# Optimization experiments

Measured on AMD Instinct MI355X. Metric: run time of the kernel, lower is better.

## Reference

```python
import jax, jax.numpy as jnp
import numpy as np
import math

NUM_HEADS = 16
ATTN_WIDTH = 256


def setup_inputs() -> dict:
    key = jax.random.key(0)
    ks = jax.random.split(key, 5)
    B, S, C, H = 2, 2048, 1024, 1024
    scale = 0.02
    return {
        "x": jax.random.normal(ks[0], (B, S, C), dtype=jnp.float32),
        "Wq": jax.random.normal(ks[1], (C, H), dtype=jnp.float32) * scale,
        "Wk": jax.random.normal(ks[2], (C, H), dtype=jnp.float32) * scale,
        "Wv": jax.random.normal(ks[3], (C, H), dtype=jnp.float32) * scale,
        "Wo": jax.random.normal(ks[4], (H, C), dtype=jnp.float32) * scale,
    }


def reference(x, Wq, Wk, Wv, Wo):
    B, S, C = x.shape
    H = NUM_HEADS
    dh = Wq.shape[1] // H  # head dim; Q.size(-1) in torch code

    def split_heads(t):
        # [B, S, H*dh] -> [B, H, S, dh]
        return t.reshape(B, S, H, dh).transpose(0, 2, 1, 3)

    q = split_heads(x @ Wq)
    k = split_heads(x @ Wk)
    v = split_heads(x @ Wv)

    scores = jnp.einsum("bhqd,bhkd->bhqk", q, k) / math.sqrt(dh)
    # exp-shift (first 'softmax-like' step, unnormalized)
    scores = jnp.exp(scores - jnp.max(scores, axis=-1, keepdims=True))
    # banded mask: tril(attn_width//2 - 1).triu(-(attn_width//2))
    i = jnp.arange(S)[:, None]
    j = jnp.arange(S)[None, :]
    d = j - i
    half = ATTN_WIDTH // 2
    mask = (d <= half - 1) & (d >= -half)
    scores = jnp.where(mask, scores, 0.0)
    # second softmax over the masked exp-scores (zeros contribute exp(0)=1)
    weights = jax.nn.softmax(scores, axis=-1)

    out = jnp.einsum("bhqk,bhkd->bhqd", weights, v)  # [B, H, S, dh]
    out = out.transpose(0, 2, 1, 3).reshape(B, S, H * dh)
    return out @ Wo
```

## Files before the change

### kernel.cpp

```cpp
#include <hip/hip_runtime.h>
#include <math.h>

typedef __bf16 bf16_t;
typedef bf16_t bf16x8 __attribute__((ext_vector_type(8)));
typedef bf16_t bf16x4 __attribute__((ext_vector_type(4)));
typedef float f32x4 __attribute__((ext_vector_type(4)));

constexpr int S_ = 2048;
constexpr float SCALE = 0.125f;

#define MFMA_B16(a, b, c) __builtin_amdgcn_mfma_f32_16x16x32_bf16(a, b, c, 0, 0, 0)

#define WAIT_VM0() __builtin_amdgcn_s_waitcnt(0x0F70)
#define WAIT_VM2() __builtin_amdgcn_s_waitcnt(0x0F72)
#define WAIT_VM4() __builtin_amdgcn_s_waitcnt(0x0F74)
#define BARRIER()  __builtin_amdgcn_s_barrier()

typedef __attribute__((address_space(1))) const void* as1_cvp;
typedef __attribute__((address_space(3))) void* as3_vp;

__device__ __forceinline__ void gl2lds16(const void* g, void* l)
{
    __builtin_amdgcn_global_load_lds((as1_cvp)g, (as3_vp)l, 16, 0, 0);
}

#define SRC_SWZ8(lane) ((((lane) & 3) ^ (((lane) >> 3) & 3)) * 8)
#define RD_SWZ8(quad, l15) ((((quad) ^ (((l15) >> 1) & 3))) * 8)

__global__ __launch_bounds__(256) void prep(const float* __restrict__ x,
                                            const float* __restrict__ Wq,
                                            const float* __restrict__ Wk,
                                            const float* __restrict__ Wv,
                                            const float* __restrict__ Wo,
                                            bf16_t* __restrict__ xb,
                                            bf16_t* __restrict__ Wqt,
                                            bf16_t* __restrict__ Wkt,
                                            bf16_t* __restrict__ Wvt,
                                            bf16_t* __restrict__ Wot,
                                            float* __restrict__ vsp)
{
    __shared__ float T[64][65];
    const int blk = blockIdx.x;
    const int tid = threadIdx.x;
    if (blk < 1024) {
#pragma unroll
        for (int u = 0; u < 4; ++u) {
            const int g = blk * 1024 + u * 256 + tid;
            const float4 v = ((const float4*)x)[g];
            bf16x4 o;
            o[0] = (bf16_t)v.x; o[1] = (bf16_t)v.y;
            o[2] = (bf16_t)v.z; o[3] = (bf16_t)v.w;
            *(bf16x4*)&xb[(size_t)g * 4] = o;
        }
    } else if (blk < 2048) {
        const int rem = blk - 1024;
        const int wsel = rem >> 8, t = rem & 255;
        const float* src = (wsel == 0) ? Wq : (wsel == 1) ? Wk : (wsel == 2) ? Wv : Wo;
        bf16_t* dst = (wsel == 0) ? Wqt : (wsel == 1) ? Wkt : (wsel == 2) ? Wvt : Wot;
        const int k0 = (t >> 4) * 64, n0 = (t & 15) * 64;
        const int rr = tid >> 4, c4 = (tid & 15) * 4;
#pragma unroll
        for (int u = 0; u < 4; ++u) {
            const float4 v = *(const float4*)&src[(size_t)(k0 + u * 16 + rr) * 1024 + n0 + c4];
            T[u * 16 + rr][c4 + 0] = v.x; T[u * 16 + rr][c4 + 1] = v.y;
            T[u * 16 + rr][c4 + 2] = v.z; T[u * 16 + rr][c4 + 3] = v.w;
        }
        __syncthreads();
#pragma unroll
        for (int u = 0; u < 4; ++u) {
            bf16x4 o;
#pragma unroll
            for (int e = 0; e < 4; ++e) o[e] = (bf16_t)T[c4 + e][u * 16 + rr];
            *(bf16x4*)&dst[(size_t)(n0 + u * 16 + rr) * 1024 + k0 + c4] = o;
        }
    } else {
#pragma unroll
        for (int u = 0; u < 8; ++u) vsp[u * 256 + tid] = 0.f;
    }
}

template <int MODE>
__device__ __forceinline__ void mfma_gemm_body(bf16_t* __restrict__ As,
                                               bf16_t* __restrict__ Bs,
                                               const bf16_t* __restrict__ A,
                                               const bf16_t* __restrict__ Bt,
                                               void* __restrict__ dst,
                                               float* __restrict__ vsum_out,
                                               int m0, int n0)
{
    const int tid = threadIdx.x;
    const int lane = tid & 63, wid = tid >> 6;
    const int l15 = lane & 15, quad = lane >> 4;
    const int wm = (wid & 1) * 64, wn = (wid >> 1) * 64;

    const int srow = wid * 32 + (lane >> 2);
    const int scg8 = SRC_SWZ8(lane);
    const bf16_t* Ag0 = A  + (size_t)(m0 + srow) * 1024 + scg8;
    const bf16_t* Ag1 = A  + (size_t)(m0 + srow + 16) * 1024 + scg8;
    const bf16_t* Bg0 = Bt + (size_t)(n0 + srow) * 1024 + scg8;
    const bf16_t* Bg1 = Bt + (size_t)(n0 + srow + 16) * 1024 + scg8;

    const int rs = RD_SWZ8(quad, l15);

    f32x4 acc[4][4];
#pragma unroll
    for (int i = 0; i < 4; ++i)
#pragma unroll
        for (int j = 0; j < 4; ++j) acc[i][j] = (f32x4){0.f, 0.f, 0.f, 0.f};

#pragma unroll
    for (int p = 0; p < 2; ++p) {
        const int k0 = p * 32;
        gl2lds16(Ag0 + k0, As + p * 4096 + (wid * 2 + 0) * 512);
        gl2lds16(Ag1 + k0, As + p * 4096 + (wid * 2 + 1) * 512);
        gl2lds16(Bg0 + k0, Bs + p * 4096 + (wid * 2 + 0) * 512);
        gl2lds16(Bg1 + k0, Bs + p * 4096 + (wid * 2 + 1) * 512);
    }

#pragma unroll
    for (int it = 0; it < 32; ++it) {
        if (it < 30) WAIT_VM4(); else WAIT_VM0();
        BARRIER();
        if (it < 30) {
            const int k0 = (it + 2) * 32;
            const int sb = (it + 2) % 3;
            gl2lds16(Ag0 + k0, As + sb * 4096 + (wid * 2 + 0) * 512);
            gl2lds16(Ag1 + k0, As + sb * 4096 + (wid * 2 + 1) * 512);
            gl2lds16(Bg0 + k0, Bs + sb * 4096 + (wid * 2 + 0) * 512);
            gl2lds16(Bg1 + k0, Bs + sb * 4096 + (wid * 2 + 1) * 512);
        }
        const int cb = it % 3;
        bf16x8 af[4], bfr[4];
#pragma unroll
        for (int mt = 0; mt < 4; ++mt)
            af[mt] = *(const bf16x8*)&As[cb * 4096 + (wm + mt * 16 + l15) * 32 + rs];
#pragma unroll
        for (int nt = 0; nt < 4; ++nt)
            bfr[nt] = *(const bf16x8*)&Bs[cb * 4096 + (wn + nt * 16 + l15) * 32 + rs];
#pragma unroll
        for (int mt = 0; mt < 4; ++mt)
#pragma unroll
            for (int nt = 0; nt < 4; ++nt)
                acc[mt][nt] = MFMA_B16(bfr[nt], af[mt], acc[mt][nt]);
    }

#pragma unroll
    for (int mt = 0; mt < 4; ++mt) {
        const int m = m0 + wm + mt * 16 + l15;
#pragma unroll
        for (int nt = 0; nt < 4; ++nt) {
            const int nb = n0 + wn + nt * 16 + quad * 4;
            if (MODE == 0) {
                *(f32x4*)&((float*)dst)[(size_t)m * 1024 + nb] = acc[mt][nt];
            } else if (MODE == 1) {
                const int bb = m >> 11, s = m & 2047;
                const int hh = nb >> 6, d = nb & 63;
                bf16x4 o;
#pragma unroll
                for (int u = 0; u < 4; ++u) o[u] = (bf16_t)acc[mt][nt][u];
                *(bf16x4*)&((bf16_t*)dst)[((size_t)(bb * 16 + hh) * 2048 + s) * 64 + d] = o;
            } else {
                const int bb = n0 >> 11;
                const int hh = m >> 6, dd = m & 63;
                bf16x4 o;
#pragma unroll
                for (int u = 0; u < 4; ++u) o[u] = (bf16_t)acc[mt][nt][u];
                *(bf16x4*)&((bf16_t*)dst)[((size_t)(bb * 16 + hh) * 64 + dd) * 2048 + (nb & 2047)] = o;
            }
        }
    }

    if (MODE == 2 && vsum_out != nullptr) {
        const int bb = n0 >> 11;
#pragma unroll
        for (int mt = 0; mt < 4; ++mt) {
            float p = 0.f;
#pragma unroll
            for (int nt = 0; nt < 4; ++nt)
                p += acc[mt][nt][0] + acc[mt][nt][1] + acc[mt][nt][2] + acc[mt][nt][3];
            p += __shfl_xor(p, 16);
            p += __shfl_xor(p, 32);
            if (quad == 0) {
                const int m = m0 + wm + mt * 16 + l15;
                atomicAdd(&vsum_out[(bb * 16 + (m >> 6)) * 64 + (m & 63)], p);
            }
        }
    }
}

__device__ __forceinline__ int remap_m(void) { return (blockIdx.x << 2) + (blockIdx.y >> 3); }
__device__ __forceinline__ int remap_n(void) { return blockIdx.y & 7; }

__global__ __launch_bounds__(256) void gemm_qkv_mfma(const bf16_t* __restrict__ xb,
                                                     const bf16_t* __restrict__ Wqt,
                                                     const bf16_t* __restrict__ Wkt,
                                                     const bf16_t* __restrict__ Wvt,
                                                     bf16_t* Qh, bf16_t* Kh, bf16_t* VhT,
                                                     float* vsp)
{
    __shared__ bf16_t As[12288];
    __shared__ bf16_t Bs[12288];
    if (blockIdx.z == 2) {
        mfma_gemm_body<2>(As, Bs, Wvt, xb, VhT, vsp, remap_n() * 128, remap_m() * 128);
    } else {
        const bf16_t* Bt = (blockIdx.z == 0) ? Wqt : Wkt;
        bf16_t* dst = (blockIdx.z == 0) ? Qh : Kh;
        mfma_gemm_body<1>(As, Bs, xb, Bt, dst, nullptr, remap_m() * 128, remap_n() * 128);
    }
}

__global__ __launch_bounds__(256) void gemm_out_mfma(const bf16_t* __restrict__ attn,
                                                     const bf16_t* __restrict__ Wot,
                                                     float* __restrict__ out)
{
    __shared__ bf16_t As[12288];
    __shared__ bf16_t Bs[12288];
    mfma_gemm_body<0>(As, Bs, attn, Wot, out, nullptr, remap_m() * 128, remap_n() * 128);
}

__global__ __launch_bounds__(256) void attn_k(const bf16_t* __restrict__ Qh,
                                              const bf16_t* __restrict__ Kh,
                                              const bf16_t* __restrict__ VhT,
                                              const float* __restrict__ vsp,
                                              bf16_t* __restrict__ attn)
{
    __shared__ bf16_t Qs[8192];
    __shared__ float mr_sh[128];
    __shared__ __align__(16) char uni[35328];

    float*  msh = (float*)uni;
    bf16_t* Ks2 = (bf16_t*)uni;
    bf16_t* VtL = (bf16_t*)(uni + 8192);
    bf16_t* Ws  = (bf16_t*)(uni + 16384);
    float*  zsh = (float*)(uni + 34816);

    const int tid = threadIdx.x;
    const int lane = tid & 63, wid = tid >> 6;
    const int l15 = lane & 15, quad = lane >> 4;

    const int f = blockIdx.x;
    const int seq = f >> 3;
    const int bh = (f & 7) + 8 * (seq >> 4);
    const int i0 = (seq & 15) * 128;
    const int b = bh >> 4, h = bh & 15;
    const bf16_t* Qb  = Qh  + (size_t)bh * 131072;
    const bf16_t* Kb  = Kh  + (size_t)bh * 131072;
    const bf16_t* VbT = VhT + (size_t)bh * 131072;

    const int ssw = SRC_SWZ8(lane);
    const int rs  = RD_SWZ8(quad, l15);

#pragma unroll
    for (int c = 0; c < 4; ++c) {
        const int gg = wid * 4 + c;
        const int half = gg >> 3;
        const int row = (gg & 7) * 16 + (lane >> 2);
        gl2lds16(Qb + (size_t)(i0 + row) * 64 + half * 32 + ssw, Qs + gg * 512);
    }
    __syncthreads();

    bf16x8 af[8][2];
#pragma unroll
    for (int mt = 0; mt < 8; ++mt)
#pragma unroll
        for (int ks = 0; ks < 2; ++ks)
            af[mt][ks] = *(const bf16x8*)&Qs[ks * 4096 + (mt * 16 + l15) * 32 + rs];

    float vm[8];
#pragma unroll
    for (int mt = 0; mt < 8; ++mt) vm[mt] = -3.0e38f;

    const bf16_t* kf0 = Kb + (size_t)(wid * 16 + l15) * 64 + quad * 8;
    bf16x8 k0 = *(const bf16x8*)(kf0);
    bf16x8 k1 = *(const bf16x8*)(kf0 + 32);

    for (int jc = 0; jc < 32; ++jc) {
        const bf16_t* pn = kf0 + (size_t)((jc < 31) ? (jc + 1) : 31) * 4096;
        const bf16x8 n0 = *(const bf16x8*)(pn);
        const bf16x8 n1 = *(const bf16x8*)(pn + 32);
        __builtin_amdgcn_s_setprio(1);
#pragma unroll
        for (int mt = 0; mt < 8; ++mt) {
            f32x4 t = (f32x4){0.f, 0.f, 0.f, 0.f};
            t = MFMA_B16(k0, af[mt][0], t);
            t = MFMA_B16(k1, af[mt][1], t);
            const float u = fmaxf(fmaxf(t[0], t[1]), t[2]);
            vm[mt] = fmaxf(fmaxf(u, t[3]), vm[mt]);
        }
        __builtin_amdgcn_s_setprio(0);
        k0 = n0; k1 = n1;
    }

#pragma unroll
    for (int mt = 0; mt < 8; ++mt) {
        float v = vm[mt];
        v = fmaxf(v, __shfl_xor(v, 16));
        v = fmaxf(v, __shfl_xor(v, 32));
        if (quad == 0) msh[(wid * 8 + mt) * 16 + l15] = v;
    }
    __syncthreads();

    if (tid < 128) {
        const int mt = tid >> 4, il = tid & 15;
        const float v = fmaxf(fmaxf(msh[(0 * 8 + mt) * 16 + il], msh[(1 * 8 + mt) * 16 + il]),
                              fmaxf(msh[(2 * 8 + mt) * 16 + il], msh[(3 * 8 + mt) * 16 + il]));
        mr_sh[tid] = v * SCALE;
    }
    __syncthreads();

    bf16x8 aq[2][2];
#pragma unroll
    for (int t = 0; t < 2; ++t)
#pragma unroll
        for (int ks = 0; ks < 2; ++ks)
            aq[t][ks] = *(const bf16x8*)&Qs[ks * 4096 + ((wid * 2 + t) * 16 + l15) * 32 + rs];

    float mreg[2][4];
#pragma unroll
    for (int t = 0; t < 2; ++t)
#pragma unroll
        for (int r = 0; r < 4; ++r)
            mreg[t][r] = mr_sh[(wid * 2 + t) * 16 + quad * 4 + r];

    f32x4 vsd4[4];
#pragma unroll
    for (int dt = 0; dt < 4; ++dt)
        vsd4[dt] = *(const f32x4*)&vsp[bh * 64 + dt * 16 + quad * 4];

    f32x4 accO[2][4];
#pragma unroll
    for (int t = 0; t < 2; ++t)
#pragma unroll
        for (int dt = 0; dt < 4; ++dt) accO[t][dt] = (f32x4){0.f, 0.f, 0.f, 0.f};
    float zp[2][4] = {{0.f, 0.f, 0.f, 0.f}, {0.f, 0.f, 0.f, 0.f}};

    for (int cb2 = 0; cb2 < 6; ++cb2) {
        const int jb = i0 - 128 + cb2 * 64;
        if (jb < 0 || jb >= S_) continue;

        __syncthreads();
#pragma unroll
        for (int c = 0; c < 2; ++c) {
            const int gg = wid * 2 + c;
            const int half = gg >> 2;
            const int row = (gg & 3) * 16 + (lane >> 2);
            gl2lds16(Kb + (size_t)(jb + row) * 64 + half * 32 + ssw, Ks2 + gg * 512);
        }
#pragma unroll
        for (int c = 0; c < 2; ++c) {
            const int gg = wid * 2 + c;
            const int d = gg * 8 + (lane >> 3);
            const int jl = (lane & 7) ^ ((lane >> 3) & 7);
            gl2lds16(VbT + (size_t)d * 2048 + jb + jl * 8, VtL + gg * 512);
        }
        __syncthreads();

#pragma unroll
        for (int t = 0; t < 2; ++t) {
            const int mt = wid * 2 + t;
#pragma unroll
            for (int jt4 = 0; jt4 < 4; ++jt4) {
                const bf16x8 kk0 = *(const bf16x8*)&Ks2[(jt4 * 16 + l15) * 32 + rs];
                const bf16x8 kk1 = *(const bf16x8*)&Ks2[2048 + (jt4 * 16 + l15) * 32 + rs];
                f32x4 sc = (f32x4){0.f, 0.f, 0.f, 0.f};
                sc = MFMA_B16(aq[t][0], kk0, sc);
                sc = MFMA_B16(aq[t][1], kk1, sc);
#pragma unroll
                for (int r = 0; r < 4; ++r) {
                    const int ig = i0 + mt * 16 + quad * 4 + r;
                    const int jg = jb + jt4 * 16 + l15;
                    const int dd = jg - ig;
                    const bool ok = (dd >= -128) && (dd <= 127);
                    const float e1 = __expf(sc[r] * SCALE - mreg[t][r]);
                    const float wv = ok ? (__expf(e1) - 1.0f) : 0.0f;
                    const bf16_t wb = (bf16_t)wv;
                    zp[t][r] += (float)wb;
                    Ws[(mt * 16 + quad * 4 + r) * 72 + jt4 * 16 + l15] = wb;
                }
            }
        }
        __syncthreads();

#pragma unroll
        for (int ks = 0; ks < 2; ++ks) {
            bf16x8 bv[4];
#pragma unroll
            for (int dt = 0; dt < 4; ++dt)
                bv[dt] = *(const bf16x8*)&VtL[(dt * 16 + l15) * 64 +
                                              (((ks * 4 + quad) ^ (l15 & 7)) * 8)];
#pragma unroll
            for (int t = 0; t < 2; ++t) {
                const int mt = wid * 2 + t;
                const bf16x8 aw = *(const bf16x8*)&Ws[(mt * 16 + l15) * 72 + ks * 32 + quad * 8];
#pragma unroll
                for (int dt = 0; dt < 4; ++dt)
                    accO[t][dt] = MFMA_B16(bv[dt], aw, accO[t][dt]);
            }
        }
    }

#pragma unroll
    for (int t = 0; t < 2; ++t)
#pragma unroll
        for (int r = 0; r < 4; ++r) {
            float z = zp[t][r];
            z += __shfl_xor(z, 1);
            z += __shfl_xor(z, 2);
            z += __shfl_xor(z, 4);
            z += __shfl_xor(z, 8);
            if (l15 == 0) zsh[wid * 32 + t * 16 + quad * 4 + r] = z + (float)S_;
        }
    __syncthreads();

#pragma unroll
    for (int t = 0; t < 2; ++t) {
        const float rz = 1.0f / zsh[wid * 32 + t * 16 + l15];
        const int irow = i0 + (wid * 2 + t) * 16 + l15;
#pragma unroll
        for (int dt = 0; dt < 4; ++dt) {
            bf16x4 o;
#pragma unroll
            for (int r = 0; r < 4; ++r)
                o[r] = (bf16_t)((accO[t][dt][r] + vsd4[dt][r]) * rz);
            *(bf16x4*)&attn[(size_t)(b * S_ + irow) * 1024 + h * 64 + dt * 16 + quad * 4] = o;
        }
    }
}

extern "C" void kernel_launch(void* const* d_in, const int* in_sizes, int n_in,
                              void* d_out, int out_size, void* d_ws, size_t ws_size,
                              hipStream_t stream)
{
    const float* x  = (const float*)d_in[0];
    const float* Wq = (const float*)d_in[1];
    const float* Wk = (const float*)d_in[2];
    const float* Wv = (const float*)d_in[3];
    const float* Wo = (const float*)d_in[4];
    float* out = (float*)d_out;

    char* ws = (char*)d_ws;
    bf16_t* xb   = (bf16_t*)(ws + 0);
    bf16_t* Wqt  = (bf16_t*)(ws + 8388608);
    bf16_t* Wkt  = (bf16_t*)(ws + 10485760);
    bf16_t* Wvt  = (bf16_t*)(ws + 12582912);
    bf16_t* Wot  = (bf16_t*)(ws + 14680064);
    bf16_t* Qh   = (bf16_t*)(ws + 16777216);
    bf16_t* Kh   = (bf16_t*)(ws + 25165824);
    bf16_t* VhT  = (bf16_t*)(ws + 33554432);
    bf16_t* attn = (bf16_t*)(ws + 41943040);
    float*  vsp  = (float*)(ws + 50331648);

    prep<<<2049, 256, 0, stream>>>(x, Wq, Wk, Wv, Wo, xb, Wqt, Wkt, Wvt, Wot, vsp);
    gemm_qkv_mfma<<<dim3(8, 32, 3), 256, 0, stream>>>(xb, Wqt, Wkt, Wvt, Qh, Kh, VhT, vsp);
    attn_k<<<512, 256, 0, stream>>>(Qh, Kh, VhT, vsp, attn);
    gemm_out_mfma<<<dim3(8, 32), 256, 0, stream>>>(attn, Wot, out);
}
```

Before: 173.7 us.

## Read K and V tiles straight from global memory in attention loop

The attention kernel no longer stages K and transposed-V tiles into shared memory with global_load_lds. Each wave now loads its MFMA operands directly from global memory, which lets the two block-wide barriers per key block go and shrinks the shared-memory footprint to just the per-wave weight tile. It also raises wave priority around the P·V MFMA section. The trade-off is that every wave re-fetches the same K/V data through the caches, and load latency is no longer hidden behind a staged copy.

```diff
diff --git a/kernel.cpp b/kernel.cpp
--- a/kernel.cpp
+++ b/kernel.cpp
@@ -12,7 +12,6 @@
 #define MFMA_B16(a, b, c) __builtin_amdgcn_mfma_f32_16x16x32_bf16(a, b, c, 0, 0, 0)
 
 #define WAIT_VM0() __builtin_amdgcn_s_waitcnt(0x0F70)
-#define WAIT_VM2() __builtin_amdgcn_s_waitcnt(0x0F72)
 #define WAIT_VM4() __builtin_amdgcn_s_waitcnt(0x0F74)
 #define BARRIER()  __builtin_amdgcn_s_barrier()
 
@@ -226,13 +225,11 @@
 {
     __shared__ bf16_t Qs[8192];
     __shared__ float mr_sh[128];
-    __shared__ __align__(16) char uni[35328];
+    __shared__ __align__(16) char uni[18944];
 
     float*  msh = (float*)uni;
-    bf16_t* Ks2 = (bf16_t*)uni;
-    bf16_t* VtL = (bf16_t*)(uni + 8192);
-    bf16_t* Ws  = (bf16_t*)(uni + 16384);
-    float*  zsh = (float*)(uni + 34816);
+    bf16_t* Ws  = (bf16_t*)uni;
+    float*  zsh = (float*)(uni + 18432);
 
     const int tid = threadIdx.x;
     const int lane = tid & 63, wid = tid >> 6;
@@ -338,30 +335,14 @@
         const int jb = i0 - 128 + cb2 * 64;
         if (jb < 0 || jb >= S_) continue;
 
-        __syncthreads();
-#pragma unroll
-        for (int c = 0; c < 2; ++c) {
-            const int gg = wid * 2 + c;
-            const int half = gg >> 2;
-            const int row = (gg & 3) * 16 + (lane >> 2);
-            gl2lds16(Kb + (size_t)(jb + row) * 64 + half * 32 + ssw, Ks2 + gg * 512);
-        }
-#pragma unroll
-        for (int c = 0; c < 2; ++c) {
-            const int gg = wid * 2 + c;
-            const int d = gg * 8 + (lane >> 3);
-            const int jl = (lane & 7) ^ ((lane >> 3) & 7);
-            gl2lds16(VbT + (size_t)d * 2048 + jb + jl * 8, VtL + gg * 512);
-        }
-        __syncthreads();
-
 #pragma unroll
         for (int t = 0; t < 2; ++t) {
             const int mt = wid * 2 + t;
 #pragma unroll
             for (int jt4 = 0; jt4 < 4; ++jt4) {
-                const bf16x8 kk0 = *(const bf16x8*)&Ks2[(jt4 * 16 + l15) * 32 + rs];
-                const bf16x8 kk1 = *(const bf16x8*)&Ks2[2048 + (jt4 * 16 + l15) * 32 + rs];
+                const bf16_t* kp = Kb + (size_t)(jb + jt4 * 16 + l15) * 64 + quad * 8;
+                const bf16x8 kk0 = *(const bf16x8*)(kp);
+                const bf16x8 kk1 = *(const bf16x8*)(kp + 32);
                 f32x4 sc = (f32x4){0.f, 0.f, 0.f, 0.f};
                 sc = MFMA_B16(aq[t][0], kk0, sc);
                 sc = MFMA_B16(aq[t][1], kk1, sc);
@@ -379,15 +360,15 @@
                 }
             }
         }
-        __syncthreads();
-
+
+        __builtin_amdgcn_s_setprio(1);
 #pragma unroll
         for (int ks = 0; ks < 2; ++ks) {
             bf16x8 bv[4];
 #pragma unroll
             for (int dt = 0; dt < 4; ++dt)
-                bv[dt] = *(const bf16x8*)&VtL[(dt * 16 + l15) * 64 +
-                                              (((ks * 4 + quad) ^ (l15 & 7)) * 8)];
+                bv[dt] = *(const bf16x8*)(VbT + (size_t)(dt * 16 + l15) * 2048
+                                          + jb + ks * 32 + quad * 8);
 #pragma unroll
             for (int t = 0; t < 2; ++t) {
                 const int mt = wid * 2 + t;
@@ -397,6 +378,7 @@
                     accO[t][dt] = MFMA_B16(bv[dt], aw, accO[t][dt]);
             }
         }
+        __builtin_amdgcn_s_setprio(0);
     }
 
 #pragma unroll
```

Result: slower. 189.9 us (+9.4%).
